# Performance work log

Measured on AMD Instinct MI355X. Metric: run time of the kernel, lower is better.

Reference implementation:

```python
import jax, jax.numpy as jnp
import numpy as np

H, W = 2048, 4096
NUM_FRAMES, NUM_CAMERAS = 200, 4


def setup_inputs() -> dict:
    key = jax.random.key(0)
    k0, k1, k2, k3, k4 = jax.random.split(key, 5)
    exposure_params = 0.1 * jax.random.normal(k0, (NUM_FRAMES,), dtype=jnp.float32)
    vignetting_params = 0.05 * jax.random.normal(k1, (NUM_CAMERAS, 3, 5), dtype=jnp.float32)
    color_params = 0.05 * jax.random.normal(k2, (NUM_FRAMES, 8), dtype=jnp.float32)
    crf_params = 0.1 * jax.random.normal(k3, (NUM_CAMERAS, 3, 4), dtype=jnp.float32)
    rgb_in = jax.random.uniform(k4, (H, W, 3), dtype=jnp.float32)
    xs = jnp.arange(W, dtype=jnp.float32) + 0.5  # pixel-center x
    ys = jnp.arange(H, dtype=jnp.float32) + 0.5  # pixel-center y
    gx, gy = jnp.meshgrid(xs, ys)  # each [H, W]
    pixel_coords = jnp.stack([gx, gy], axis=-1)  # [H, W, 2] (x, y)
    return {
        'exposure_params': exposure_params,
        'vignetting_params': vignetting_params,
        'color_params': color_params,
        'crf_params': crf_params,
        'rgb_in': rgb_in,
        'pixel_coords': pixel_coords,
        'resolution_w': W,
        'resolution_h': H,
        'camera_idx': 1,
        'frame_idx': 3,
    }


def _ppisp_forward(exposure_params, vignetting_params, color_params, crf_params,
                   rgb_flat, coords_flat, resolution_w, resolution_h,
                   camera_idx, frame_idx):
    # rgb_flat: [N, 3], coords_flat: [N, 2]
    rgb = rgb_flat
    # --- stage 1: per-frame exposure scale ---
    if frame_idx >= 0:
        rgb = rgb * jnp.exp(exposure_params[frame_idx])
    # --- stage 2: per-camera radial vignetting polynomial (per channel) ---
    if camera_idx >= 0:
        vp = vignetting_params[camera_idx]  # [3, 5] = (cx, cy, a1, a2, a3) per channel
        cx = (0.5 + vp[:, 0]) * resolution_w   # [3] optical center x in pixels
        cy = (0.5 + vp[:, 1]) * resolution_h   # [3]
        norm2 = (0.5 * resolution_w) ** 2 + (0.5 * resolution_h) ** 2
        dx = coords_flat[:, :1] - cx           # [N, 3]
        dy = coords_flat[:, 1:] - cy           # [N, 3]
        r2 = (dx * dx + dy * dy) / norm2       # normalized squared radius
        vig = 1.0 + r2 * (vp[:, 2] + r2 * (vp[:, 3] + r2 * vp[:, 4]))  # Horner cubic in r^2
        rgb = rgb * vig
    # --- stage 3: per-frame 8-param color correction (identity-anchored 3x3) ---
    if frame_idx >= 0:
        p = color_params[frame_idx]  # [8]
        one = jnp.ones((), dtype=p.dtype)
        M = jnp.stack([
            jnp.stack([one + p[0], p[1], p[2]]),
            jnp.stack([p[3], one + p[4], p[5]]),
            jnp.stack([p[6], p[7], one]),
        ])  # [3, 3]
        rgb = rgb @ M.T
    # --- stage 4: per-camera CRF gamma curve (per channel, 4 params) ---
    if camera_idx >= 0:
        q = crf_params[camera_idx]      # [3, 4] = (log_gamma, b1, b2, b3)
        gamma = jnp.exp(q[:, 0])        # [3]
        x = jnp.clip(rgb, 0.0, 1.0)
        y = x ** gamma
        # smooth perturbation anchored at y=0 and y=1
        y = y + y * (1.0 - y) * (q[:, 1] + q[:, 2] * y + q[:, 3] * (1.0 - y))
        rgb = y
    return rgb


def reference(exposure_params, vignetting_params, color_params, crf_params,
              rgb_in, pixel_coords, resolution_w, resolution_h, camera_idx, frame_idx):
    original_shape = rgb_in.shape
    rgb_flat = rgb_in.reshape(-1, 3).astype(jnp.float32)
    coords_flat = pixel_coords.reshape(-1, 2).astype(jnp.float32)
    out = _ppisp_forward(exposure_params.astype(jnp.float32),
                         vignetting_params.astype(jnp.float32),
                         color_params.astype(jnp.float32),
                         crf_params.astype(jnp.float32),
                         rgb_flat, coords_flat,
                         int(resolution_w), int(resolution_h),
                         int(camera_idx), int(frame_idx))
    return out.reshape(original_shape)
```

## Files before the change

kernel.cpp:

```cpp
#include <hip/hip_runtime.h>
#include <math.h>

constexpr int W = 4096;
constexpr int H = 2048;
constexpr int W_SHIFT = 12;
constexpr int NPIX = W * H;
constexpr int NFLOAT = NPIX * 3;
constexpr int BLOCK = 256;
constexpr int WAVES = BLOCK / 64;
constexpr int PIX_PER_LANE = 4;
constexpr int FLT_PER_LANE = 3 * PIX_PER_LANE;
constexpr int CHUNK_FLT = 64 * FLT_PER_LANE;
constexpr int CHUNK_PIX = CHUNK_FLT / 3;
constexpr int CHUNKS = NFLOAT / CHUNK_FLT;
constexpr int GRID = 2048;
constexpr int C = CHUNKS / (GRID * WAVES);

#define AS1 __attribute__((address_space(1)))
#define AS3 __attribute__((address_space(3)))

__global__ __launch_bounds__(BLOCK) void ppisp_kernel(
    const float* __restrict__ exposure,
    const float* __restrict__ vigp,
    const float* __restrict__ colorp,
    const float* __restrict__ crfp,
    const float* __restrict__ rgb_in,
    const int*   __restrict__ cam_idx,
    const int*   __restrict__ frm_idx,
    float*       __restrict__ out)
{
    __shared__ float smem[WAVES][2][CHUNK_FLT];

    const int t    = threadIdx.x;
    const int wave = t >> 6;
    const int lane = t & 63;

    const int wc0 = blockIdx.x * (WAVES * C) + wave * C;

    const int cam = __builtin_amdgcn_readfirstlane(cam_idx[0]);
    const int frm = __builtin_amdgcn_readfirstlane(frm_idx[0]);

    const float escale = (frm >= 0) ? __expf(exposure[frm]) : 1.0f;

    float cx[3], cy[3], a1[3], a2[3], a3[3];
    if (cam >= 0) {
        const float* vp = vigp + cam * 15;
        #pragma unroll
        for (int c = 0; c < 3; ++c) {
            cx[c] = (0.5f + vp[c * 5 + 0]) * (float)W;
            cy[c] = (0.5f + vp[c * 5 + 1]) * (float)H;
            a1[c] = vp[c * 5 + 2];
            a2[c] = vp[c * 5 + 3];
            a3[c] = vp[c * 5 + 4];
        }
    } else {
        #pragma unroll
        for (int c = 0; c < 3; ++c) {
            cx[c] = cy[c] = 0.0f;
            a1[c] = a2[c] = a3[c] = 0.0f;
        }
    }
    const float nx = 0.5f * (float)W, ny = 0.5f * (float)H;
    const float inv_norm2 = 1.0f / (nx * nx + ny * ny);

    float M[9];
    if (frm >= 0) {
        const float* p = colorp + frm * 8;
        M[0] = 1.0f + p[0]; M[1] = p[1];        M[2] = p[2];
        M[3] = p[3];        M[4] = 1.0f + p[4]; M[5] = p[5];
        M[6] = p[6];        M[7] = p[7];        M[8] = 1.0f;
    } else {
        M[0] = 1.0f; M[1] = 0.0f; M[2] = 0.0f;
        M[3] = 0.0f; M[4] = 1.0f; M[5] = 0.0f;
        M[6] = 0.0f; M[7] = 0.0f; M[8] = 1.0f;
    }

    float gam[3], b1[3], b2[3], b3[3];
    const int crf_on = (cam >= 0);
    if (crf_on) {
        const float* q = crfp + cam * 12;
        #pragma unroll
        for (int c = 0; c < 3; ++c) {
            gam[c] = __expf(q[c * 4 + 0]);
            b1[c]  = q[c * 4 + 1];
            b2[c]  = q[c * 4 + 2];
            b3[c]  = q[c * 4 + 3];
        }
    } else {
        #pragma unroll
        for (int c = 0; c < 3; ++c) { gam[c] = 1.0f; b1[c] = b2[c] = b3[c] = 0.0f; }
    }

    asm volatile("s_waitcnt vmcnt(0)" ::: "memory");

    {
        const size_t f0 = (size_t)wc0 * CHUNK_FLT;
        #pragma unroll
        for (int j = 0; j < 3; ++j) {
            __builtin_amdgcn_global_load_lds(
                (const AS1 void*)(rgb_in + f0 + j * 256 + lane * 4),
                (AS3 void*)&smem[wave][0][j * 256], 16, 0, 0);
        }
    }

    #pragma unroll
    for (int i = 0; i < C; ++i) {
        const int cbuf = i & 1;

        if (i + 1 < C) {
            const size_t fn = (size_t)(wc0 + i + 1) * CHUNK_FLT;
            #pragma unroll
            for (int j = 0; j < 3; ++j) {
                __builtin_amdgcn_global_load_lds(
                    (const AS1 void*)(rgb_in + fn + j * 256 + lane * 4),
                    (AS3 void*)&smem[wave][cbuf ^ 1][j * 256], 16, 0, 0);
            }
        }

        if (i == 0 || i == C - 1) {
            asm volatile("s_waitcnt vmcnt(3)" ::: "memory");
        } else {
            asm volatile("s_waitcnt vmcnt(6)" ::: "memory");
        }
        __builtin_amdgcn_sched_barrier(0);

        float4* sb = (float4*)smem[wave][cbuf];
        const float4 x0 = sb[lane * 3 + 0];
        const float4 x1 = sb[lane * 3 + 1];
        const float4 x2 = sb[lane * 3 + 2];

        float v[FLT_PER_LANE];
        v[0] = x0.x; v[1]  = x0.y; v[2]  = x0.z; v[3]  = x0.w;
        v[4] = x1.x; v[5]  = x1.y; v[6]  = x1.z; v[7]  = x1.w;
        v[8] = x2.x; v[9]  = x2.y; v[10] = x2.z; v[11] = x2.w;

        const int pb = (wc0 + i) * CHUNK_PIX + lane * PIX_PER_LANE;
        #pragma unroll
        for (int k = 0; k < PIX_PER_LANE; ++k) {
            const int p = pb + k;
            const float px = (float)(p & (W - 1)) + 0.5f;
            const float py = (float)(p >> W_SHIFT) + 0.5f;

            float ch[3];
            #pragma unroll
            for (int c = 0; c < 3; ++c) ch[c] = v[k * 3 + c] * escale;

            #pragma unroll
            for (int c = 0; c < 3; ++c) {
                const float dx = px - cx[c];
                const float dy = py - cy[c];
                const float r2 = (dx * dx + dy * dy) * inv_norm2;
                ch[c] *= 1.0f + r2 * (a1[c] + r2 * (a2[c] + r2 * a3[c]));
            }

            float o[3];
            o[0] = M[0] * ch[0] + M[1] * ch[1] + M[2] * ch[2];
            o[1] = M[3] * ch[0] + M[4] * ch[1] + M[5] * ch[2];
            o[2] = M[6] * ch[0] + M[7] * ch[1] + M[8] * ch[2];

            if (crf_on) {
                #pragma unroll
                for (int c = 0; c < 3; ++c) {
                    const float x = fminf(fmaxf(o[c], 0.0f), 1.0f);
                    float y = exp2f(gam[c] * __log2f(x));
                    y = y + y * (1.0f - y) * (b1[c] + b2[c] * y + b3[c] * (1.0f - y));
                    o[c] = y;
                }
            }

            v[k * 3 + 0] = o[0];
            v[k * 3 + 1] = o[1];
            v[k * 3 + 2] = o[2];
        }

        sb[lane * 3 + 0] = make_float4(v[0], v[1], v[2],  v[3]);
        sb[lane * 3 + 1] = make_float4(v[4], v[5], v[6],  v[7]);
        sb[lane * 3 + 2] = make_float4(v[8], v[9], v[10], v[11]);

        {
            const float4* sl = (const float4*)smem[wave][cbuf];
            float4* og = (float4*)(out + (size_t)(wc0 + i) * CHUNK_FLT);
            #pragma unroll
            for (int j = 0; j < 3; ++j)
                og[j * 64 + lane] = sl[j * 64 + lane];
        }
    }
}

extern "C" void kernel_launch(void* const* d_in, const int* in_sizes, int n_in,
                              void* d_out, int out_size, void* d_ws, size_t ws_size,
                              hipStream_t stream) {
    const float* exposure = (const float*)d_in[0];
    const float* vigp     = (const float*)d_in[1];
    const float* colorp   = (const float*)d_in[2];
    const float* crfp     = (const float*)d_in[3];
    const float* rgb_in   = (const float*)d_in[4];
    const int* cam_idx = (const int*)d_in[8];
    const int* frm_idx = (const int*)d_in[9];
    float* out = (float*)d_out;

    ppisp_kernel<<<dim3(GRID), dim3(BLOCK), 0, stream>>>(
        exposure, vigp, colorp, crfp, rgb_in, cam_idx, frm_idx, out);
}
```

Before: 229.6 us.

## Use one chunk per wave with a large grid instead of a persistent double-buffered loop

Result: no change. 228.2 us (-0.6%).

```diff
diff --git a/kernel.cpp b/kernel.cpp
--- a/kernel.cpp
+++ b/kernel.cpp
@@ -12,9 +12,7 @@
 constexpr int FLT_PER_LANE = 3 * PIX_PER_LANE;
 constexpr int CHUNK_FLT = 64 * FLT_PER_LANE;
 constexpr int CHUNK_PIX = CHUNK_FLT / 3;
-constexpr int CHUNKS = NFLOAT / CHUNK_FLT;
-constexpr int GRID = 2048;
-constexpr int C = CHUNKS / (GRID * WAVES);
+constexpr int GRID = NPIX / (WAVES * CHUNK_PIX);
 
 #define AS1 __attribute__((address_space(1)))
 #define AS3 __attribute__((address_space(3)))
@@ -29,16 +27,24 @@
     const int*   __restrict__ frm_idx,
     float*       __restrict__ out)
 {
-    __shared__ float smem[WAVES][2][CHUNK_FLT];
+    __shared__ float smem[WAVES][CHUNK_FLT];
 
     const int t    = threadIdx.x;
     const int wave = t >> 6;
     const int lane = t & 63;
 
-    const int wc0 = blockIdx.x * (WAVES * C) + wave * C;
+    const int chunk = blockIdx.x * WAVES + wave;
+    const size_t f0 = (size_t)chunk * CHUNK_FLT;
 
-    const int cam = __builtin_amdgcn_readfirstlane(cam_idx[0]);
-    const int frm = __builtin_amdgcn_readfirstlane(frm_idx[0]);
+    #pragma unroll
+    for (int j = 0; j < 3; ++j) {
+        __builtin_amdgcn_global_load_lds(
+            (const AS1 void*)(rgb_in + f0 + j * 256 + lane * 4),
+            (AS3 void*)&smem[wave][j * 256], 16, 0, 0);
+    }
+
+    const int cam = cam_idx[0];
+    const int frm = frm_idx[0];
 
     const float escale = (frm >= 0) ? __expf(exposure[frm]) : 1.0f;
 
@@ -92,99 +98,61 @@
     }
 
     asm volatile("s_waitcnt vmcnt(0)" ::: "memory");
+    __builtin_amdgcn_sched_barrier(0);
 
-    {
-        const size_t f0 = (size_t)wc0 * CHUNK_FLT;
+    const float4* sb = (const float4*)smem[wave];
+    const float4 x0 = sb[lane * 3 + 0];
+    const float4 x1 = sb[lane * 3 + 1];
+    const float4 x2 = sb[lane * 3 + 2];
+
+    float v[FLT_PER_LANE];
+    v[0] = x0.x; v[1]  = x0.y; v[2]  = x0.z; v[3]  = x0.w;
+    v[4] = x1.x; v[5]  = x1.y; v[6]  = x1.z; v[7]  = x1.w;
+    v[8] = x2.x; v[9]  = x2.y; v[10] = x2.z; v[11] = x2.w;
+
+    const int pb = chunk * CHUNK_PIX + lane * PIX_PER_LANE;
+    #pragma unroll
+    for (int k = 0; k < PIX_PER_LANE; ++k) {
+        const int p = pb + k;
+        const float px = (float)(p & (W - 1)) + 0.5f;
+        const float py = (float)(p >> W_SHIFT) + 0.5f;
+
+        float ch[3];
         #pragma unroll
-        for (int j = 0; j < 3; ++j) {
-            __builtin_amdgcn_global_load_lds(
-                (const AS1 void*)(rgb_in + f0 + j * 256 + lane * 4),
-                (AS3 void*)&smem[wave][0][j * 256], 16, 0, 0);
+        for (int c = 0; c < 3; ++c) ch[c] = v[k * 3 + c] * escale;
+
+        #pragma unroll
+        for (int c = 0; c < 3; ++c) {
+            const float dx = px - cx[c];
+            const float dy = py - cy[c];
+            const float r2 = (dx * dx + dy * dy) * inv_norm2;
+            ch[c] *= 1.0f + r2 * (a1[c] + r2 * (a2[c] + r2 * a3[c]));
         }
-    }
 
-    #pragma unroll
-    for (int i = 0; i < C; ++i) {
-        const int cbuf = i & 1;
+        float o[3];
+        o[0] = M[0] * ch[0] + M[1] * ch[1] + M[2] * ch[2];
+        o[1] = M[3] * ch[0] + M[4] * ch[1] + M[5] * ch[2];
+        o[2] = M[6] * ch[0] + M[7] * ch[1] + M[8] * ch[2];
 
-        if (i + 1 < C) {
-            const size_t fn = (size_t)(wc0 + i + 1) * CHUNK_FLT;
+        if (crf_on) {
             #pragma unroll
-            for (int j = 0; j < 3; ++j) {
-                __builtin_amdgcn_global_load_lds(
-                    (const AS1 void*)(rgb_in + fn + j * 256 + lane * 4),
-                    (AS3 void*)&smem[wave][cbuf ^ 1][j * 256], 16, 0, 0);
+            for (int c = 0; c < 3; ++c) {
+                const float x = fminf(fmaxf(o[c], 0.0f), 1.0f);
+                float y = exp2f(gam[c] * __log2f(x));
+                y = y + y * (1.0f - y) * (b1[c] + b2[c] * y + b3[c] * (1.0f - y));
+                o[c] = y;
             }
         }
 
-        if (i == 0 || i == C - 1) {
-            asm volatile("s_waitcnt vmcnt(3)" ::: "memory");
-        } else {
-            asm volatile("s_waitcnt vmcnt(6)" ::: "memory");
-        }
-        __builtin_amdgcn_sched_barrier(0);
+        v[k * 3 + 0] = o[0];
+        v[k * 3 + 1] = o[1];
+        v[k * 3 + 2] = o[2];
+    }
 
-        float4* sb = (float4*)smem[wave][cbuf];
-        const float4 x0 = sb[lane * 3 + 0];
-        const float4 x1 = sb[lane * 3 + 1];
-        const float4 x2 = sb[lane * 3 + 2];
-
-        float v[FLT_PER_LANE];
-        v[0] = x0.x; v[1]  = x0.y; v[2]  = x0.z; v[3]  = x0.w;
-        v[4] = x1.x; v[5]  = x1.y; v[6]  = x1.z; v[7]  = x1.w;
-        v[8] = x2.x; v[9]  = x2.y; v[10] = x2.z; v[11] = x2.w;
-
-        const int pb = (wc0 + i) * CHUNK_PIX + lane * PIX_PER_LANE;
-        #pragma unroll
-        for (int k = 0; k < PIX_PER_LANE; ++k) {
-            const int p = pb + k;
-            const float px = (float)(p & (W - 1)) + 0.5f;
-            const float py = (float)(p >> W_SHIFT) + 0.5f;
-
-            float ch[3];
-            #pragma unroll
-            for (int c = 0; c < 3; ++c) ch[c] = v[k * 3 + c] * escale;
-
-            #pragma unroll
-            for (int c = 0; c < 3; ++c) {
-                const float dx = px - cx[c];
-                const float dy = py - cy[c];
-                const float r2 = (dx * dx + dy * dy) * inv_norm2;
-                ch[c] *= 1.0f + r2 * (a1[c] + r2 * (a2[c] + r2 * a3[c]));
-            }
-
-            float o[3];
-            o[0] = M[0] * ch[0] + M[1] * ch[1] + M[2] * ch[2];
-            o[1] = M[3] * ch[0] + M[4] * ch[1] + M[5] * ch[2];
-            o[2] = M[6] * ch[0] + M[7] * ch[1] + M[8] * ch[2];
-
-            if (crf_on) {
-                #pragma unroll
-                for (int c = 0; c < 3; ++c) {
-                    const float x = fminf(fmaxf(o[c], 0.0f), 1.0f);
-                    float y = exp2f(gam[c] * __log2f(x));
-                    y = y + y * (1.0f - y) * (b1[c] + b2[c] * y + b3[c] * (1.0f - y));
-                    o[c] = y;
-                }
-            }
-
-            v[k * 3 + 0] = o[0];
-            v[k * 3 + 1] = o[1];
-            v[k * 3 + 2] = o[2];
-        }
-
-        sb[lane * 3 + 0] = make_float4(v[0], v[1], v[2],  v[3]);
-        sb[lane * 3 + 1] = make_float4(v[4], v[5], v[6],  v[7]);
-        sb[lane * 3 + 2] = make_float4(v[8], v[9], v[10], v[11]);
-
-        {
-            const float4* sl = (const float4*)smem[wave][cbuf];
-            float4* og = (float4*)(out + (size_t)(wc0 + i) * CHUNK_FLT);
-            #pragma unroll
-            for (int j = 0; j < 3; ++j)
-                og[j * 64 + lane] = sl[j * 64 + lane];
-        }
-    }
+    float4* og = (float4*)(out + f0 + (size_t)lane * FLT_PER_LANE);
+    og[0] = make_float4(v[0], v[1], v[2],  v[3]);
+    og[1] = make_float4(v[4], v[5], v[6],  v[7]);
+    og[2] = make_float4(v[8], v[9], v[10], v[11]);
 }
 
 extern "C" void kernel_launch(void* const* d_in, const int* in_sizes, int n_in,
```
